# Kernel tuning notes

Measured on AMD Instinct MI355X. Metric: run time of the kernel, lower is better.

Reference implementation:

```python
import jax, jax.numpy as jnp
import numpy as np

B, R, N, E, DIN, DOUT = 2, 2, 50000, 500000, 128, 128


def setup_inputs() -> dict:
    key = jax.random.key(0)
    k_x, k_src, k_dst, k_val, k_w = jax.random.split(key, 5)
    x = jax.random.normal(k_x, (B, N, DIN), dtype=jnp.float32)
    edge_src = jax.random.randint(k_src, (B, R, E), 0, N, dtype=jnp.int32)
    edge_dst = jax.random.randint(k_dst, (B, R, E), 0, N, dtype=jnp.int32)
    edge_val = jax.random.uniform(k_val, (B, R, E), dtype=jnp.float32)
    # Glorot-uniform init as in init_weight: range = sqrt(6/(fan_in+fan_out))
    init_range = float(np.sqrt(6.0 / (DIN + DOUT)))
    weights = jax.random.uniform(k_w, (R, DIN, DOUT), minval=-init_range,
                                 maxval=init_range, dtype=jnp.float32)
    bias = jnp.zeros((DOUT,), dtype=jnp.float32)
    return {"x": x, "edge_val": edge_val, "weights": weights, "bias": bias,
            "edge_src": edge_src, "edge_dst": edge_dst}


def reference(x, edge_val, weights, bias, edge_src, edge_dst):
    # Dense feature transform per relation: pre_sup = x @ W_r  -> [B, R, N, DOUT]
    pre = jnp.einsum('bnd,rde->brne', x, weights)
    bi = jnp.arange(B)[:, None, None]   # [B,1,1]
    ri = jnp.arange(R)[None, :, None]   # [1,R,1]
    # Sparse adjacency matmul A_r @ pre_sup:
    # out[dst] += A[dst, src] * pre_sup[src]  (edge list form)
    msgs = edge_val[..., None] * pre[bi, ri, edge_src]          # [B,R,E,DOUT]
    agg = jnp.zeros((B, R, N, DOUT), dtype=pre.dtype)
    agg = agg.at[bi, ri, edge_dst].add(msgs)                    # scatter-add
    # Sum across relations (tf.add_n), add bias, relu activation
    out = agg.sum(axis=1) + bias                                # [B,N,DOUT]
    return jax.nn.relu(out)
```

## Files before the change

kernel.cpp:

```cpp
#include <hip/hip_runtime.h>

#define BB 2
#define RR 2
#define NN 50000
#define EE 500000
#define DD 128
#define NSLOT 4
#define BSH 6
#define BSZ 64
#define NB 782
#define FT 8192
#define FBLK 62
#define SCAP 2048
#define DSTR 50048

#define C_XB   0u
#define C_REC  25600000u
#define C_CNT  33600000u
#define C_OFS  33612512u
#define C_CUR  33625056u
#define C_DOF  33637568u
#define C_WT   34438336u
#define C_TOTAL 34503872u

#define A_XB   0u
#define A_REC  12800000u
#define A_CNT  20800000u
#define A_OFS  20812544u
#define A_CUR  20825088u
#define A_DOF  20837632u
#define A_WT   21638400u

typedef __attribute__((ext_vector_type(8))) short bf16x8;
typedef __attribute__((ext_vector_type(4))) float f32x4;

__device__ __forceinline__ unsigned short f2bf(float f) {
    unsigned int u = __float_as_uint(f);
    u += 0x7fffu + ((u >> 16) & 1u);
    return (unsigned short)(u >> 16);
}

__device__ __forceinline__ bf16x8 pack8(float4 a, float4 b) {
    bf16x8 r;
    r[0] = (short)f2bf(a.x); r[1] = (short)f2bf(a.y);
    r[2] = (short)f2bf(a.z); r[3] = (short)f2bf(a.w);
    r[4] = (short)f2bf(b.x); r[5] = (short)f2bf(b.y);
    r[6] = (short)f2bf(b.z); r[7] = (short)f2bf(b.w);
    return r;
}

__global__ __launch_bounds__(256) void wprep_kernel(
    const float* __restrict__ w, unsigned short* __restrict__ wt2)
{
    int idx = blockIdx.x * 256 + threadIdx.x;
    if (idx >= RR * DD * DD) return;
    int r = idx >> 14;
    int k = (idx >> 7) & (DD - 1);
    int n = idx & (DD - 1);
    wt2[(size_t)n * 256 + r * DD + k] = f2bf(w[idx]);
}

__global__ __launch_bounds__(256) void cast_kernel(
    const float* __restrict__ x, unsigned short* __restrict__ xb)
{
    const size_t bo = (size_t)blockIdx.y * NN * DD;
    int i8 = (blockIdx.x * 256 + threadIdx.x) * 8;
    if (i8 >= NN * DD) return;
    float4 v0 = *(const float4*)&x[bo + i8];
    float4 v1 = *(const float4*)&x[bo + i8 + 4];
    *(bf16x8*)&xb[bo + i8] = pack8(v0, v1);
}

__global__ __launch_bounds__(256) void hist_kernel(
    const int* __restrict__ edst, int* __restrict__ counts)
{
    __shared__ int h[NB];
    for (int i = threadIdx.x; i < NB; i += 256) h[i] = 0;
    __syncthreads();
    const int slot = blockIdx.y;
    const int* ed = edst + (size_t)slot * EE;
    for (int e = blockIdx.x * 256 + threadIdx.x; e < EE; e += 128 * 256)
        atomicAdd(&h[ed[e] >> BSH], 1);
    __syncthreads();
    int* c = counts + slot * NB;
    for (int i = threadIdx.x; i < NB; i += 256) {
        int v = h[i];
        if (v) atomicAdd(&c[i], v);
    }
}

__global__ __launch_bounds__(1024) void scan_kernel(
    const int* __restrict__ counts, int* __restrict__ offsets,
    int* __restrict__ cursor)
{
    __shared__ int s[1024];
    const int slot = blockIdx.x;
    int v = (threadIdx.x < NB) ? counts[slot * NB + threadIdx.x] : 0;
    s[threadIdx.x] = v;
    for (int o = 1; o < 1024; o <<= 1) {
        __syncthreads();
        int t = (threadIdx.x >= o) ? s[threadIdx.x - o] : 0;
        __syncthreads();
        s[threadIdx.x] += t;
    }
    __syncthreads();
    if (threadIdx.x < NB) {
        int incl = s[threadIdx.x];
        offsets[slot * 784 + threadIdx.x + 1] = incl;
        cursor[slot * NB + threadIdx.x] = incl - v;
    }
    if (threadIdx.x == 0) offsets[slot * 784] = 0;
}

__global__ __launch_bounds__(1024) void fill_kernel(
    const int* __restrict__ esrc, const int* __restrict__ edst,
    const float* __restrict__ ev, int* __restrict__ cursor,
    unsigned int* __restrict__ recs)
{
    __shared__ int lh[NB];
    __shared__ int lbase[NB];
    const int slot = blockIdx.y;
    const size_t eb = (size_t)slot * EE;
    const int e0 = blockIdx.x * FT;

    for (int i = threadIdx.x; i < NB; i += 1024) lh[i] = 0;
    __syncthreads();
    for (int t = 0; t < FT; t += 1024) {
        int e = e0 + t + threadIdx.x;
        if (e < EE) atomicAdd(&lh[edst[eb + e] >> BSH], 1);
    }
    __syncthreads();
    for (int i = threadIdx.x; i < NB; i += 1024) {
        int c = lh[i];
        lbase[i] = c ? atomicAdd(&cursor[slot * NB + i], c) : 0;
        lh[i] = 0;
    }
    __syncthreads();
    for (int t = 0; t < FT; t += 1024) {
        int e = e0 + t + threadIdx.x;
        if (e < EE) {
            int d = edst[eb + e];
            int bk = d >> BSH;
            unsigned vq = (unsigned)__builtin_rintf(ev[eb + e] * 1023.0f);
            unsigned rec = (unsigned)esrc[eb + e] |
                           ((unsigned)(d & (BSZ - 1)) << 16) | (vq << 22);
            int p = lbase[bk] + atomicAdd(&lh[bk], 1);
            recs[eb + p] = rec;
        }
    }
}

#define DEQ (1.0f / 1023.0f)

__global__ __launch_bounds__(256) void sort_kernel(
    unsigned int* __restrict__ recs, const int* __restrict__ offsets,
    int* __restrict__ dofs)
{
    __shared__ unsigned int lrec[SCAP];
    __shared__ int cnt[BSZ];
    __shared__ int cur[BSZ];
    const int bk = blockIdx.x, slot = blockIdx.y;
    unsigned int* rp = recs + (size_t)slot * EE;
    const int s = offsets[slot * 784 + bk], e = offsets[slot * 784 + bk + 1];
    const int n = e - s;

    for (int i = threadIdx.x; i < n; i += 256) lrec[i] = rp[s + i];
    if (threadIdx.x < BSZ) cnt[threadIdx.x] = 0;
    __syncthreads();
    for (int i = threadIdx.x; i < n; i += 256)
        atomicAdd(&cnt[(lrec[i] >> 16) & (BSZ - 1)], 1);
    __syncthreads();
    if (threadIdx.x < 64) {
        int v = cnt[threadIdx.x];
        int incl = v;
        #pragma unroll
        for (int o = 1; o < 64; o <<= 1) {
            int t = __shfl_up(incl, o, 64);
            if (threadIdx.x >= o) incl += t;
        }
        int excl = incl - v;
        cur[threadIdx.x] = excl;
        dofs[(size_t)slot * DSTR + bk * BSZ + threadIdx.x] = s + excl;
    }
    __syncthreads();
    for (int i = threadIdx.x; i < n; i += 256) {
        unsigned r = lrec[i];
        int p = atomicAdd(&cur[(r >> 16) & (BSZ - 1)], 1);
        float v = (float)(r >> 22) * DEQ;
        rp[s + p] = (r & 0xffffu) | ((unsigned)f2bf(v) << 16);
    }
}

#define LO16(u) __uint_as_float((u) << 16)
#define HI16(u) __uint_as_float((u) & 0xffff0000u)

__device__ __forceinline__ void gacc(const unsigned short* __restrict__ xb,
                                     const unsigned int* __restrict__ rp,
                                     unsigned i, unsigned e, unsigned lane2,
                                     float& acc0, float& acc1)
{
    for (; i + 8 <= e; i += 8) {
        unsigned q[8], u[8];
        #pragma unroll
        for (int j = 0; j < 8; ++j) q[j] = rp[i + j];
        #pragma unroll
        for (int j = 0; j < 8; ++j)
            u[j] = *(const unsigned*)(xb + (((q[j] & 0xffffu) << 7) + lane2));
        #pragma unroll
        for (int j = 0; j < 8; ++j) {
            float s = __uint_as_float(q[j] & 0xffff0000u);
            acc0 = fmaf(s, LO16(u[j]), acc0);
            acc1 = fmaf(s, HI16(u[j]), acc1);
        }
    }
    if (i + 4 <= e) {
        unsigned q[4], u[4];
        #pragma unroll
        for (int j = 0; j < 4; ++j) q[j] = rp[i + j];
        #pragma unroll
        for (int j = 0; j < 4; ++j)
            u[j] = *(const unsigned*)(xb + (((q[j] & 0xffffu) << 7) + lane2));
        #pragma unroll
        for (int j = 0; j < 4; ++j) {
            float s = __uint_as_float(q[j] & 0xffff0000u);
            acc0 = fmaf(s, LO16(u[j]), acc0);
            acc1 = fmaf(s, HI16(u[j]), acc1);
        }
        i += 4;
    }
    for (; i < e; ++i) {
        unsigned q0 = rp[i];
        unsigned u0 = *(const unsigned*)(xb + (((q0 & 0xffffu) << 7) + lane2));
        float s0 = __uint_as_float(q0 & 0xffff0000u);
        acc0 = fmaf(s0, LO16(u0), acc0); acc1 = fmaf(s0, HI16(u0), acc1);
    }
}

__global__ __launch_bounds__(256) void gather_dual_kernel(
    const unsigned short* __restrict__ xb,
    const unsigned int* __restrict__ recs,
    const int* __restrict__ dofs,
    float* __restrict__ out)
{
    const int y = blockIdx.y;
    const unsigned short* xbb = xb + (size_t)y * NN * DD;
    const unsigned int* rp0 = recs + (size_t)(y * 2) * EE;
    const unsigned int* rp1 = rp0 + EE;
    const int* d0p = dofs + (size_t)(y * 2) * DSTR;
    const int* d1p = d0p + DSTR;
    unsigned short* agg = (unsigned short*)(out + (size_t)y * NN * DD);

    const int d = blockIdx.x * 4 + (threadIdx.x >> 6);
    const unsigned lane2 = (threadIdx.x & 63) * 2;

    float a0 = 0.f, a1 = 0.f, b0 = 0.f, b1 = 0.f;
    gacc(xbb, rp0, d0p[d], d0p[d + 1], lane2, a0, a1);
    gacc(xbb, rp1, d1p[d], d1p[d + 1], lane2, b0, b1);

    unsigned short* row = agg + (size_t)d * 256;
    unsigned p0 = (unsigned)f2bf(a0) | ((unsigned)f2bf(a1) << 16);
    unsigned p1 = (unsigned)f2bf(b0) | ((unsigned)f2bf(b1) << 16);
    *(unsigned*)(row + lane2) = p0;
    *(unsigned*)(row + DD + lane2) = p1;
}

__global__ __launch_bounds__(256) void gemm_agg_kernel(
    const unsigned short* __restrict__ wt2,
    const float* __restrict__ bias,
    float* __restrict__ out)
{
    float* outb = out + (size_t)blockIdx.y * NN * DD;
    const unsigned short* agg = (const unsigned short*)outb;
    const int tid = threadIdx.x;
    const int w = tid >> 6, lane = tid & 63;
    const int wr = w >> 1, wc = w & 1;
    const int lq = lane >> 4, lr = lane & 15;
    const int row0 = blockIdx.x * 128;

    f32x4 acc[4][4] = {};

    #pragma unroll
    for (int ks = 0; ks < 8; ++ks) {
        const int k0 = ks * 32 + lq * 8;
        bf16x8 a[4], b[4];
        #pragma unroll
        for (int mi = 0; mi < 4; ++mi) {
            int row = row0 + wr * 64 + mi * 16 + lr;
            bf16x8 v = {};
            if (row < NN) v = *(const bf16x8*)(agg + (size_t)row * 256 + k0);
            a[mi] = v;
        }
        #pragma unroll
        for (int ni = 0; ni < 4; ++ni) {
            int n = wc * 64 + ni * 16 + lr;
            b[ni] = *(const bf16x8*)(wt2 + (size_t)n * 256 + k0);
        }
        #pragma unroll
        for (int mi = 0; mi < 4; ++mi)
            #pragma unroll
            for (int ni = 0; ni < 4; ++ni)
                acc[mi][ni] = __builtin_amdgcn_mfma_f32_16x16x32_bf16(
                    a[mi], b[ni], acc[mi][ni], 0, 0, 0);
    }

    __syncthreads();

    #pragma unroll
    for (int mi = 0; mi < 4; ++mi) {
        #pragma unroll
        for (int q = 0; q < 4; ++q) {
            int row = row0 + wr * 64 + mi * 16 + lq * 4 + q;
            if (row < NN) {
                #pragma unroll
                for (int ni = 0; ni < 4; ++ni) {
                    int col = wc * 64 + ni * 16 + lr;
                    outb[(size_t)row * DD + col] =
                        fmaxf(acc[mi][ni][q] + bias[col], 0.f);
                }
            }
        }
    }
}

extern "C" void kernel_launch(void* const* d_in, const int* in_sizes, int n_in,
                              void* d_out, int out_size, void* d_ws, size_t ws_size,
                              hipStream_t stream) {
    const float* x     = (const float*)d_in[0];
    const float* eval_ = (const float*)d_in[1];
    const float* w     = (const float*)d_in[2];
    const float* bias  = (const float*)d_in[3];
    const int*   esrc  = (const int*)d_in[4];
    const int*   edst  = (const int*)d_in[5];
    float* out = (float*)d_out;

    const bool useC = (ws_size >= (size_t)C_TOTAL);

    char* ws = (char*)d_ws;
    unsigned short* xb      = (unsigned short*)(ws + (useC ? C_XB : A_XB));
    unsigned int*   recs    = (unsigned int*)(ws + (useC ? C_REC : A_REC));
    int*            counts  = (int*)(ws + (useC ? C_CNT : A_CNT));
    int*            offsets = (int*)(ws + (useC ? C_OFS : A_OFS));
    int*            cursor  = (int*)(ws + (useC ? C_CUR : A_CUR));
    int*            dofs    = (int*)(ws + (useC ? C_DOF : A_DOF));
    unsigned short* wt2     = (unsigned short*)(ws + (useC ? C_WT : A_WT));

    const dim3 blk(256);
    const dim3 cast_grid((NN * DD / 8 + 255) / 256);
    const dim3 gath_grid(NN / 4);
    const dim3 gemm_grid((NN + 127) / 128);

    hipMemsetAsync(counts, 0, NSLOT * NB * sizeof(int), stream);
    wprep_kernel<<<(RR * DD * DD + 255) / 256, blk, 0, stream>>>(w, wt2);

    hist_kernel<<<dim3(128, NSLOT), blk, 0, stream>>>(edst, counts);
    scan_kernel<<<dim3(NSLOT), dim3(1024), 0, stream>>>(counts, offsets, cursor);
    fill_kernel<<<dim3(FBLK, NSLOT), dim3(1024), 0, stream>>>(
        esrc, edst, eval_, cursor, recs);
    sort_kernel<<<dim3(NB, NSLOT), blk, 0, stream>>>(recs, offsets, dofs);

    if (useC) {
        cast_kernel<<<dim3(cast_grid.x, BB), blk, 0, stream>>>(x, xb);
        gather_dual_kernel<<<dim3(gath_grid.x, BB), blk, 0, stream>>>(
            xb, recs, dofs, out);
        gemm_agg_kernel<<<dim3(gemm_grid.x, BB), blk, 0, stream>>>(
            wt2, bias, out);
    } else {
        for (int b = 0; b < BB; ++b) {
            cast_kernel<<<cast_grid, blk, 0, stream>>>(
                x + (size_t)b * NN * DD, xb);
            gather_dual_kernel<<<gath_grid, blk, 0, stream>>>(
                xb, recs + (size_t)(b * 2) * EE, dofs + (size_t)(b * 2) * DSTR,
                out + (size_t)b * NN * DD);
            gemm_agg_kernel<<<gemm_grid, blk, 0, stream>>>(
                wt2, bias, out + (size_t)b * NN * DD);
        }
    }
}
```

Baseline: 184.2 us.

## Fuse histogram, cast and weight prep into one kernel; split gather edges across half-waves

Merges the destination histogram, the bf16 cast of x and the weight transpose into a single prep kernel, whose blocks branch on block index, so three launches and their serialization gaps become one. The gather kernel now has each half-wave handle alternate edges with 8-byte loads covering four features. The two halves are combined with a cross-lane shuffle, and each half writes one relation's row. This trades more bytes per load and fewer edges per lane for extra shuffle and tail-handling work.

```diff
diff --git a/kernel.cpp b/kernel.cpp
--- a/kernel.cpp
+++ b/kernel.cpp
@@ -13,6 +13,7 @@
 #define FBLK 62
 #define SCAP 2048
 #define DSTR 50048
+#define CASTB 3125
 
 #define C_XB   0u
 #define C_REC  25600000u
@@ -47,6 +48,41 @@
     r[4] = (short)f2bf(b.x); r[5] = (short)f2bf(b.y);
     r[6] = (short)f2bf(b.z); r[7] = (short)f2bf(b.w);
     return r;
+}
+
+__global__ __launch_bounds__(256) void prep_kernel(
+    const float* __restrict__ x, unsigned short* __restrict__ xb,
+    const int* __restrict__ edst, int* __restrict__ counts,
+    const float* __restrict__ w, unsigned short* __restrict__ wt2)
+{
+    __shared__ int h[NB];
+    const int blk = blockIdx.x;
+    const int tid = threadIdx.x;
+    if (blk < 512) {
+        for (int i = tid; i < NB; i += 256) h[i] = 0;
+        __syncthreads();
+        const int slot = blk >> 7;
+        const int* ed = edst + (size_t)slot * EE;
+        for (int e = (blk & 127) * 256 + tid; e < EE; e += 128 * 256)
+            atomicAdd(&h[ed[e] >> BSH], 1);
+        __syncthreads();
+        int* c = counts + slot * NB;
+        for (int i = tid; i < NB; i += 256) {
+            int v = h[i];
+            if (v) atomicAdd(&c[i], v);
+        }
+    } else if (blk < 512 + 2 * CASTB) {
+        const size_t i8 = (size_t)(blk - 512) * 2048 + (size_t)tid * 8;
+        float4 v0 = *(const float4*)&x[i8];
+        float4 v1 = *(const float4*)&x[i8 + 4];
+        *(bf16x8*)&xb[i8] = pack8(v0, v1);
+    } else {
+        int idx = (blk - 512 - 2 * CASTB) * 256 + tid;
+        int r = idx >> 14;
+        int k = (idx >> 7) & (DD - 1);
+        int n = idx & (DD - 1);
+        wt2[(size_t)n * 256 + r * DD + k] = f2bf(w[idx]);
+    }
 }
 
 __global__ __launch_bounds__(256) void wprep_kernel(
@@ -194,45 +230,45 @@
 #define LO16(u) __uint_as_float((u) << 16)
 #define HI16(u) __uint_as_float((u) & 0xffff0000u)
 
-__device__ __forceinline__ void gacc(const unsigned short* __restrict__ xb,
-                                     const unsigned int* __restrict__ rp,
-                                     unsigned i, unsigned e, unsigned lane2,
-                                     float& acc0, float& acc1)
+__device__ __forceinline__ void gacc2(const unsigned short* __restrict__ xb,
+                                      const unsigned int* __restrict__ rp,
+                                      unsigned i, unsigned e,
+                                      unsigned half, unsigned lane4,
+                                      float acc[4])
 {
     for (; i + 8 <= e; i += 8) {
-        unsigned q[8], u[8];
-        #pragma unroll
-        for (int j = 0; j < 8; ++j) q[j] = rp[i + j];
-        #pragma unroll
-        for (int j = 0; j < 8; ++j)
-            u[j] = *(const unsigned*)(xb + (((q[j] & 0xffffu) << 7) + lane2));
-        #pragma unroll
-        for (int j = 0; j < 8; ++j) {
-            float s = __uint_as_float(q[j] & 0xffff0000u);
-            acc0 = fmaf(s, LO16(u[j]), acc0);
-            acc1 = fmaf(s, HI16(u[j]), acc1);
-        }
-    }
-    if (i + 4 <= e) {
-        unsigned q[4], u[4];
-        #pragma unroll
-        for (int j = 0; j < 4; ++j) q[j] = rp[i + j];
+        unsigned q[4]; uint2 u[4];
+        #pragma unroll
+        for (int j = 0; j < 4; ++j) q[j] = rp[i + 2 * j + half];
         #pragma unroll
         for (int j = 0; j < 4; ++j)
-            u[j] = *(const unsigned*)(xb + (((q[j] & 0xffffu) << 7) + lane2));
+            u[j] = *(const uint2*)(xb + (((q[j] & 0xffffu) << 7) + lane4));
         #pragma unroll
         for (int j = 0; j < 4; ++j) {
             float s = __uint_as_float(q[j] & 0xffff0000u);
-            acc0 = fmaf(s, LO16(u[j]), acc0);
-            acc1 = fmaf(s, HI16(u[j]), acc1);
-        }
-        i += 4;
-    }
-    for (; i < e; ++i) {
-        unsigned q0 = rp[i];
-        unsigned u0 = *(const unsigned*)(xb + (((q0 & 0xffffu) << 7) + lane2));
-        float s0 = __uint_as_float(q0 & 0xffff0000u);
-        acc0 = fmaf(s0, LO16(u0), acc0); acc1 = fmaf(s0, HI16(u0), acc1);
+            acc[0] = fmaf(s, LO16(u[j].x), acc[0]);
+            acc[1] = fmaf(s, HI16(u[j].x), acc[1]);
+            acc[2] = fmaf(s, LO16(u[j].y), acc[2]);
+            acc[3] = fmaf(s, HI16(u[j].y), acc[3]);
+        }
+    }
+    for (; i + 2 <= e; i += 2) {
+        unsigned q = rp[i + half];
+        uint2 u = *(const uint2*)(xb + (((q & 0xffffu) << 7) + lane4));
+        float s = __uint_as_float(q & 0xffff0000u);
+        acc[0] = fmaf(s, LO16(u.x), acc[0]);
+        acc[1] = fmaf(s, HI16(u.x), acc[1]);
+        acc[2] = fmaf(s, LO16(u.y), acc[2]);
+        acc[3] = fmaf(s, HI16(u.y), acc[3]);
+    }
+    if (i < e && half == 0) {
+        unsigned q = rp[i];
+        uint2 u = *(const uint2*)(xb + (((q & 0xffffu) << 7) + lane4));
+        float s = __uint_as_float(q & 0xffff0000u);
+        acc[0] = fmaf(s, LO16(u.x), acc[0]);
+        acc[1] = fmaf(s, HI16(u.x), acc[1]);
+        acc[2] = fmaf(s, LO16(u.y), acc[2]);
+        acc[3] = fmaf(s, HI16(u.y), acc[3]);
     }
 }
 
@@ -251,17 +287,29 @@
     unsigned short* agg = (unsigned short*)(out + (size_t)y * NN * DD);
 
     const int d = blockIdx.x * 4 + (threadIdx.x >> 6);
-    const unsigned lane2 = (threadIdx.x & 63) * 2;
-
-    float a0 = 0.f, a1 = 0.f, b0 = 0.f, b1 = 0.f;
-    gacc(xbb, rp0, d0p[d], d0p[d + 1], lane2, a0, a1);
-    gacc(xbb, rp1, d1p[d], d1p[d + 1], lane2, b0, b1);
-
-    unsigned short* row = agg + (size_t)d * 256;
-    unsigned p0 = (unsigned)f2bf(a0) | ((unsigned)f2bf(a1) << 16);
-    unsigned p1 = (unsigned)f2bf(b0) | ((unsigned)f2bf(b1) << 16);
-    *(unsigned*)(row + lane2) = p0;
-    *(unsigned*)(row + DD + lane2) = p1;
+    const int lane = threadIdx.x & 63;
+    const unsigned half = (unsigned)(lane >> 5);
+    const unsigned lane4 = (unsigned)(lane & 31) * 4;
+
+    float a[4] = {0.f, 0.f, 0.f, 0.f};
+    float b[4] = {0.f, 0.f, 0.f, 0.f};
+    gacc2(xbb, rp0, d0p[d], d0p[d + 1], half, lane4, a);
+    gacc2(xbb, rp1, d1p[d], d1p[d + 1], half, lane4, b);
+
+    #pragma unroll
+    for (int k = 0; k < 4; ++k) {
+        a[k] += __shfl_xor(a[k], 32);
+        b[k] += __shfl_xor(b[k], 32);
+    }
+
+    float s0 = half ? b[0] : a[0];
+    float s1 = half ? b[1] : a[1];
+    float s2 = half ? b[2] : a[2];
+    float s3 = half ? b[3] : a[3];
+    uint2 pv;
+    pv.x = (unsigned)f2bf(s0) | ((unsigned)f2bf(s1) << 16);
+    pv.y = (unsigned)f2bf(s2) | ((unsigned)f2bf(s3) << 16);
+    *(uint2*)(agg + (size_t)d * 256 + half * DD + lane4) = pv;
 }
 
 __global__ __launch_bounds__(256) void gemm_agg_kernel(
@@ -345,26 +393,32 @@
     unsigned short* wt2     = (unsigned short*)(ws + (useC ? C_WT : A_WT));
 
     const dim3 blk(256);
-    const dim3 cast_grid((NN * DD / 8 + 255) / 256);
     const dim3 gath_grid(NN / 4);
     const dim3 gemm_grid((NN + 127) / 128);
 
     hipMemsetAsync(counts, 0, NSLOT * NB * sizeof(int), stream);
-    wprep_kernel<<<(RR * DD * DD + 255) / 256, blk, 0, stream>>>(w, wt2);
-
-    hist_kernel<<<dim3(128, NSLOT), blk, 0, stream>>>(edst, counts);
-    scan_kernel<<<dim3(NSLOT), dim3(1024), 0, stream>>>(counts, offsets, cursor);
-    fill_kernel<<<dim3(FBLK, NSLOT), dim3(1024), 0, stream>>>(
-        esrc, edst, eval_, cursor, recs);
-    sort_kernel<<<dim3(NB, NSLOT), blk, 0, stream>>>(recs, offsets, dofs);
 
     if (useC) {
-        cast_kernel<<<dim3(cast_grid.x, BB), blk, 0, stream>>>(x, xb);
+        prep_kernel<<<512 + 2 * CASTB + 128, blk, 0, stream>>>(
+            x, xb, edst, counts, w, wt2);
+        scan_kernel<<<dim3(NSLOT), dim3(1024), 0, stream>>>(
+            counts, offsets, cursor);
+        fill_kernel<<<dim3(FBLK, NSLOT), dim3(1024), 0, stream>>>(
+            esrc, edst, eval_, cursor, recs);
+        sort_kernel<<<dim3(NB, NSLOT), blk, 0, stream>>>(recs, offsets, dofs);
         gather_dual_kernel<<<dim3(gath_grid.x, BB), blk, 0, stream>>>(
             xb, recs, dofs, out);
         gemm_agg_kernel<<<dim3(gemm_grid.x, BB), blk, 0, stream>>>(
             wt2, bias, out);
     } else {
+        wprep_kernel<<<(RR * DD * DD + 255) / 256, blk, 0, stream>>>(w, wt2);
+        hist_kernel<<<dim3(128, NSLOT), blk, 0, stream>>>(edst, counts);
+        scan_kernel<<<dim3(NSLOT), dim3(1024), 0, stream>>>(
+            counts, offsets, cursor);
+        fill_kernel<<<dim3(FBLK, NSLOT), dim3(1024), 0, stream>>>(
+            esrc, edst, eval_, cursor, recs);
+        sort_kernel<<<dim3(NB, NSLOT), blk, 0, stream>>>(recs, offsets, dofs);
+        const dim3 cast_grid((NN * DD / 8 + 255) / 256);
         for (int b = 0; b < BB; ++b) {
             cast_kernel<<<cast_grid, blk, 0, stream>>>(
                 x + (size_t)b * NN * DD, xb);
```

Measured after the change: 181.4 us. Within noise of the previous version (-1.6%).
